# Optimization experiments

Hardware: AMD Instinct MI355X
Metric: run time of the kernel (lower is better)

Reference implementation:

```python
import jax, jax.numpy as jnp
import numpy as np

B, N, M = 8, 8192, 2048
C1, C2 = 128, 256
H = 256  # mlp hidden/out channels


def setup_inputs() -> dict:
    key = jax.random.key(0)
    ks = jax.random.split(key, 8)
    return {
        "unknown": jax.random.normal(ks[0], (B, N, 3), dtype=jnp.float32),
        "known": jax.random.normal(ks[1], (B, M, 3), dtype=jnp.float32),
        "unknow_feats": jax.random.normal(ks[2], (B, C1, N), dtype=jnp.float32),
        "known_feats": jax.random.normal(ks[3], (B, C2, M), dtype=jnp.float32),
        "W1": jax.random.normal(ks[4], (H, C1 + C2), dtype=jnp.float32) * 0.02,
        "b1": jnp.zeros((H,), dtype=jnp.float32),
        "W2": jax.random.normal(ks[5], (H, H), dtype=jnp.float32) * 0.02,
        "b2": jnp.zeros((H,), dtype=jnp.float32),
    }


def _three_nn(unknown, known):
    # squared pairwise distances (B, n, m)
    d2 = jnp.sum((unknown[:, :, None, :] - known[:, None, :, :]) ** 2, axis=-1)
    neg_d2_top, idx = jax.lax.top_k(-d2, 3)  # 3 smallest distances
    dist = jnp.sqrt(jnp.maximum(-neg_d2_top, 0.0))  # (B, n, 3)
    return dist, idx


def _three_interpolate(features, idx, weight):
    # features: (B, c, m); idx, weight: (B, n, 3) -> (B, c, n)
    Bc, c, m = features.shape
    n = idx.shape[1]
    idx_flat = jnp.broadcast_to(idx.reshape(Bc, 1, n * 3), (Bc, c, n * 3))
    gathered = jnp.take_along_axis(features, idx_flat, axis=2).reshape(Bc, c, n, 3)
    return jnp.sum(gathered * weight[:, None, :, :], axis=-1)


def reference(unknown, known, unknow_feats, known_feats, W1, b1, W2, b2):
    dist, idx = _three_nn(unknown, known)
    dist_recip = 1.0 / (dist + 1e-8)
    weight = dist_recip / jnp.sum(dist_recip, axis=2, keepdims=True)  # (B, n, 3)
    interpolated = _three_interpolate(known_feats, idx, weight)  # (B, C2, n)
    new_features = jnp.concatenate([interpolated, unknow_feats], axis=1)  # (B, C1+C2, n)
    # shared MLP: two conv1x1 (bias, no BN) + ReLU
    h = jax.nn.relu(jnp.einsum('oc,bcn->bon', W1, new_features) + b1[None, :, None])
    out = jax.nn.relu(jnp.einsum('oc,bcn->bon', W2, h) + b2[None, :, None])
    return out
```

## Files before the change

kernel.cpp:

```cpp
#include <hip/hip_runtime.h>

using bf16x8 = __attribute__((ext_vector_type(8))) short;
using f32x4  = __attribute__((ext_vector_type(4))) float;

constexpr int Bb = 8, Nn = 8192, Mm = 2048, C1 = 128, C2 = 256, Hh = 256, K1 = 384;
constexpr int KT1 = K1 / 32;
constexpr int KT2 = Hh / 32;
constexpr int RT = Hh / 16;
constexpr int NQ = 2;
constexpr int MQ = Mm / NQ;
constexpr int PSTR = 8;

__device__ __forceinline__ short f2bf(float x) {
  union { float f; unsigned u; } v; v.f = x;
  unsigned r = v.u + 0x7fff + ((v.u >> 16) & 1);
  return (short)(r >> 16);
}

__device__ __forceinline__ unsigned pk2bf(float a, float b) {
#if defined(__has_builtin) && __has_builtin(__builtin_amdgcn_cvt_pk_bf16_f32)
  typedef __attribute__((ext_vector_type(2))) __bf16 bf2_t;
  bf2_t r = __builtin_amdgcn_cvt_pk_bf16_f32(a, b);
  union { bf2_t v; unsigned u; } cvt; cvt.v = r;
  return cvt.u;
#else
  return (unsigned)(unsigned short)f2bf(a) | ((unsigned)(unsigned short)f2bf(b) << 16);
#endif
}

__device__ __forceinline__ float bflo(unsigned d) { return __uint_as_float(d << 16); }
__device__ __forceinline__ float bfhi(unsigned d) { return __uint_as_float(d & 0xffff0000u); }

__device__ __forceinline__ void merge3(float a0, float a1, float a2, int A0, int A1, int A2,
                                       float b0, float b1, float b2, int B0, int B1, int B2,
                                       float& m0, float& m1, float& m2,
                                       int& j0, int& j1, int& j2) {
  bool ta = a0 <= b0;
  m0 = ta ? a0 : b0; j0 = ta ? A0 : B0;
  float na0 = ta ? a1 : a0, na1 = ta ? a2 : a1;
  int   nA0 = ta ? A1 : A0, nA1 = ta ? A2 : A1;
  float nb0 = ta ? b0 : b1, nb1 = ta ? b1 : b2;
  int   nB0 = ta ? B0 : B1, nB1 = ta ? B1 : B2;
  ta = na0 <= nb0;
  m1 = ta ? na0 : nb0; j1 = ta ? nA0 : nB0;
  float ma0 = ta ? na1 : na0; int mA0 = ta ? nA1 : nA0;
  float mb0 = ta ? nb0 : nb1; int mB0 = ta ? nB0 : nB1;
  ta = ma0 <= mb0;
  m2 = ta ? ma0 : mb0; j2 = ta ? mA0 : mB0;
}

__global__ __launch_bounds__(256) void prep_all_k(const float* __restrict__ kf,
                                                  short* __restrict__ kfTb,
                                                  const float* __restrict__ W1,
                                                  const float* __restrict__ W2,
                                                  short* __restrict__ W1f,
                                                  short* __restrict__ W2f) {
  __shared__ float tile[32][33];
  int bid = blockIdx.x, tid = threadIdx.x;
  if (bid < 4096) {
    int cx = bid & 63, ry = (bid >> 6) & 7, z = bid >> 9;
    const float* src = kf + (size_t)z * C2 * Mm;
    short* dst = kfTb + (size_t)z * Mm * C2;
    int c0 = cx * 32, r0 = ry * 32;
    int tx = tid & 31, ty = tid >> 5;
#pragma unroll
    for (int rr = ty; rr < 32; rr += 8)
      tile[rr][tx] = src[(size_t)(r0 + rr) * Mm + c0 + tx];
    __syncthreads();
#pragma unroll
    for (int cc = ty; cc < 32; cc += 8)
      dst[(size_t)(c0 + cc) * C2 + r0 + tx] = f2bf(tile[tx][cc]);
    return;
  }
  int id = (bid - 4096) * 256 + tid;
  const int n1 = KT1 * RT * 64;
  const int n2 = KT2 * RT * 64;
  if (id < n1) {
    int lane = id & 63, t = id >> 6;
    int kt = t / RT, rt = t % RT;
    int m = rt * 16 + (lane & 15), k0 = kt * 32 + (lane >> 4) * 8;
    bf16x8 f;
#pragma unroll
    for (int j = 0; j < 8; ++j) f[j] = f2bf(W1[(size_t)m * K1 + k0 + j]);
    *(bf16x8*)(W1f + (size_t)id * 8) = f;
  } else if (id < n1 + n2) {
    int id2 = id - n1;
    int lane = id2 & 63, t = id2 >> 6;
    int kt = t / RT, rt = t % RT;
    int m = rt * 16 + (lane & 15), k0 = kt * 32 + (lane >> 4) * 8;
    bf16x8 f;
#pragma unroll
    for (int j = 0; j < 8; ++j) f[j] = f2bf(W2[(size_t)m * Hh + k0 + j]);
    *(bf16x8*)(W2f + (size_t)id2 * 8) = f;
  }
}

__global__ __launch_bounds__(256) void nn_half_k(const float* __restrict__ unknown,
                                                 const float* __restrict__ known,
                                                 float* __restrict__ pd,
                                                 int* __restrict__ pi) {
  __shared__ float kx[MQ], ky[MQ], kz[MQ];
  int bid = blockIdx.x;
  int b = bid >> 6, rem = bid & 63;
  int q = rem & 1, nblk = rem >> 1;
  int n = nblk * 256 + threadIdx.x;
  const float* kb = known + ((size_t)b * Mm + q * MQ) * 3;
  for (int p = threadIdx.x; p < MQ; p += 256) {
    kx[p] = kb[3 * p]; ky[p] = kb[3 * p + 1]; kz[p] = kb[3 * p + 2];
  }
  __syncthreads();

  size_t ui = ((size_t)b * Nn + n) * 3;
  float ux = unknown[ui], uy = unknown[ui + 1], uz = unknown[ui + 2];
  float d0 = 1e30f, d1 = 1e30f, d2 = 1e30f;
  int i0 = 0, i1 = 0, i2 = 0;
  int gbase = q * MQ;

#define NN_STEP(xx, yy, zz, qq)                                         \
  {                                                                     \
    float dx = ux - (xx), dy = uy - (yy), dz = uz - (zz);               \
    float dd = dx * dx + dy * dy + dz * dz;                             \
    if (__any(dd < d2)) {    \
      int jm = gbase + jb + (qq);                                       \
      bool c0 = dd < d0, c1 = dd < d1, c2 = dd < d2;                    \
      d2 = c1 ? d1 : (c2 ? dd : d2); i2 = c1 ? i1 : (c2 ? jm : i2);     \
      d1 = c0 ? d0 : (c1 ? dd : d1); i1 = c0 ? i0 : (c1 ? jm : i1);     \
      d0 = c0 ? dd : d0;             i0 = c0 ? jm : i0;                 \
    }                                                                   \
  }

  for (int jb = 0; jb < MQ; jb += 4) {
    float4 xs = *(const float4*)&kx[jb];
    float4 ys = *(const float4*)&ky[jb];
    float4 zs = *(const float4*)&kz[jb];
    NN_STEP(xs.x, ys.x, zs.x, 0)
    NN_STEP(xs.y, ys.y, zs.y, 1)
    NN_STEP(xs.z, ys.z, zs.z, 2)
    NN_STEP(xs.w, ys.w, zs.w, 3)
  }
#undef NN_STEP

  size_t o = ((size_t)b * Nn + n) * PSTR + q * 4;
  *(float4*)&pd[o] = make_float4(d0, d1, d2, 0.f);
  *(int4*)&pi[o]   = make_int4(i0, i1, i2, 0);
}

__global__ __launch_bounds__(256) void fused_gemm_k(
    const float* __restrict__ uf, const short* __restrict__ kfTb,
    const short* __restrict__ W1f, const float* __restrict__ b1,
    const short* __restrict__ W2f, const float* __restrict__ b2,
    const float* __restrict__ pd, const int* __restrict__ pi,
    float* __restrict__ out) {
  __shared__ short Fs[KT1 * 4 * 64 * 8];
  short* Hs = Fs;
  int bid = blockIdx.x;
  int b = bid >> 7, bt = bid & 127;
  int tid = threadIdx.x, lane = tid & 63, wv = tid >> 6;
  int quad = lane >> 4, col = lane & 15;

  {
    int n = bt * 64 + wv * 16 + col;
    size_t pbase = (size_t)(b * Nn + n) * PSTR;
    float4 da = *(const float4*)&pd[pbase];
    float4 db = *(const float4*)&pd[pbase + 4];
    int4 ia = *(const int4*)&pi[pbase];
    int4 ib = *(const int4*)&pi[pbase + 4];
    float m0, m1, m2;
    int g0, g1, g2;
    merge3(da.x, da.y, da.z, ia.x, ia.y, ia.z,
           db.x, db.y, db.z, ib.x, ib.y, ib.z, m0, m1, m2, g0, g1, g2);
    float s0 = sqrtf(m0), s1 = sqrtf(m1), s2 = sqrtf(m2);
    float r0 = 1.f / (s0 + 1e-8f), r1 = 1.f / (s1 + 1e-8f), r2 = 1.f / (s2 + 1e-8f);
    float rs = 1.f / (r0 + r1 + r2);
    float w0 = r0 * rs, w1 = r1 * rs, w2 = r2 * rs;

    const short* kfb = kfTb + (size_t)b * Mm * C2;
#pragma unroll 4
    for (int kt = 0; kt < 8; ++kt) {
      int c0 = kt * 32 + quad * 8;
      uint4 q0 = *(const uint4*)&kfb[(size_t)g0 * C2 + c0];
      uint4 q1 = *(const uint4*)&kfb[(size_t)g1 * C2 + c0];
      uint4 q2 = *(const uint4*)&kfb[(size_t)g2 * C2 + c0];
      float e0 = w0 * bflo(q0.x) + w1 * bflo(q1.x) + w2 * bflo(q2.x);
      float e1 = w0 * bfhi(q0.x) + w1 * bfhi(q1.x) + w2 * bfhi(q2.x);
      float e2 = w0 * bflo(q0.y) + w1 * bflo(q1.y) + w2 * bflo(q2.y);
      float e3 = w0 * bfhi(q0.y) + w1 * bfhi(q1.y) + w2 * bfhi(q2.y);
      float e4 = w0 * bflo(q0.z) + w1 * bflo(q1.z) + w2 * bflo(q2.z);
      float e5 = w0 * bfhi(q0.z) + w1 * bfhi(q1.z) + w2 * bfhi(q2.z);
      float e6 = w0 * bflo(q0.w) + w1 * bflo(q1.w) + w2 * bflo(q2.w);
      float e7 = w0 * bfhi(q0.w) + w1 * bfhi(q1.w) + w2 * bfhi(q2.w);
      uint4 packed;
      packed.x = pk2bf(e0, e1); packed.y = pk2bf(e2, e3);
      packed.z = pk2bf(e4, e5); packed.w = pk2bf(e6, e7);
      *(uint4*)&Fs[((kt * 4 + wv) * 64 + lane) * 8] = packed;
    }
#pragma unroll 2
    for (int kt = 8; kt < 12; ++kt) {
      int c1 = (kt - 8) * 32 + quad * 8;
      float e[8];
#pragma unroll
      for (int j = 0; j < 8; ++j)
        e[j] = uf[((size_t)b * C1 + c1 + j) * Nn + n];
      uint4 packed;
      packed.x = pk2bf(e[0], e[1]); packed.y = pk2bf(e[2], e[3]);
      packed.z = pk2bf(e[4], e[5]); packed.w = pk2bf(e[6], e[7]);
      *(uint4*)&Fs[((kt * 4 + wv) * 64 + lane) * 8] = packed;
    }
  }
  __syncthreads();

  f32x4 acc[4][4];
#pragma unroll
  for (int r = 0; r < 4; ++r)
#pragma unroll
    for (int c = 0; c < 4; ++c) acc[r][c] = (f32x4){0.f, 0.f, 0.f, 0.f};

  for (int kt = 0; kt < KT1; ++kt) {
    bf16x8 Afr[4], Bfr[4];
#pragma unroll
    for (int r = 0; r < 4; ++r)
      Afr[r] = *(const bf16x8*)(W1f + ((size_t)(kt * RT + wv * 4 + r) * 64 + lane) * 8);
#pragma unroll
    for (int c = 0; c < 4; ++c)
      Bfr[c] = *(const bf16x8*)&Fs[((kt * 4 + c) * 64 + lane) * 8];
#pragma unroll
    for (int r = 0; r < 4; ++r)
#pragma unroll
      for (int c = 0; c < 4; ++c)
        acc[r][c] = __builtin_amdgcn_mfma_f32_16x16x32_bf16(Afr[r], Bfr[c], acc[r][c], 0, 0, 0);
  }
  __syncthreads();

#pragma unroll
  for (int r = 0; r < 4; ++r) {
    f32x4 bq = *(const f32x4*)&b1[wv * 64 + r * 16 + quad * 4];
#pragma unroll
    for (int c = 0; c < 4; ++c)
#pragma unroll
      for (int reg = 0; reg < 4; ++reg)
        acc[r][c][reg] = fmaxf(acc[r][c][reg] + bq[reg], 0.f);
  }
  {
    int addr_lo = (((quad & 1) * 2) * 16 + col) * 4;
    bool hiSel = lane >= 32;
#pragma unroll
    for (int ktl = 0; ktl < 2; ++ktl)
#pragma unroll
      for (int c = 0; c < 4; ++c) {
        float e[8];
#pragma unroll
        for (int j = 0; j < 8; ++j) {
          int addr = addr_lo + (j >> 2) * 64;
          int lo = __builtin_amdgcn_ds_bpermute(addr, __float_as_int(acc[ktl * 2][c][j & 3]));
          int hi = __builtin_amdgcn_ds_bpermute(addr, __float_as_int(acc[ktl * 2 + 1][c][j & 3]));
          e[j] = __int_as_float(hiSel ? hi : lo);
        }
        uint4 packed;
        packed.x = pk2bf(e[0], e[1]); packed.y = pk2bf(e[2], e[3]);
        packed.z = pk2bf(e[4], e[5]); packed.w = pk2bf(e[6], e[7]);
        *(uint4*)&Hs[(((wv * 2 + ktl) * 4 + c) * 64 + lane) * 8] = packed;
      }
  }
  __syncthreads();

  f32x4 acc2[4][4];
#pragma unroll
  for (int r = 0; r < 4; ++r)
#pragma unroll
    for (int c = 0; c < 4; ++c) acc2[r][c] = (f32x4){0.f, 0.f, 0.f, 0.f};

  for (int kt = 0; kt < KT2; ++kt) {
    bf16x8 Afr[4], Bfr[4];
#pragma unroll
    for (int r = 0; r < 4; ++r)
      Afr[r] = *(const bf16x8*)(W2f + ((size_t)(kt * RT + wv * 4 + r) * 64 + lane) * 8);
#pragma unroll
    for (int c = 0; c < 4; ++c)
      Bfr[c] = *(const bf16x8*)&Hs[((kt * 4 + c) * 64 + lane) * 8];
#pragma unroll
    for (int r = 0; r < 4; ++r)
#pragma unroll
      for (int c = 0; c < 4; ++c)
        acc2[r][c] = __builtin_amdgcn_mfma_f32_16x16x32_bf16(Afr[r], Bfr[c], acc2[r][c], 0, 0, 0);
  }

#pragma unroll
  for (int r = 0; r < 4; ++r) {
    f32x4 bq = *(const f32x4*)&b2[wv * 64 + r * 16 + quad * 4];
#pragma unroll
    for (int c = 0; c < 4; ++c)
#pragma unroll
      for (int reg = 0; reg < 4; ++reg) {
        int rowg = wv * 64 + r * 16 + quad * 4 + reg;
        int n = bt * 64 + c * 16 + col;
        out[((size_t)b * Hh + rowg) * Nn + n] = fmaxf(acc2[r][c][reg] + bq[reg], 0.f);
      }
  }
}

extern "C" void kernel_launch(void* const* d_in, const int* in_sizes, int n_in,
                              void* d_out, int out_size, void* d_ws, size_t ws_size,
                              hipStream_t stream) {
  const float* unknown = (const float*)d_in[0];
  const float* known   = (const float*)d_in[1];
  const float* uf      = (const float*)d_in[2];
  const float* kf      = (const float*)d_in[3];
  const float* W1      = (const float*)d_in[4];
  const float* b1      = (const float*)d_in[5];
  const float* W2      = (const float*)d_in[6];
  const float* b2      = (const float*)d_in[7];
  float* out = (float*)d_out;

  char* p = (char*)d_ws;
  short* kfTb = (short*)p; p += (size_t)Bb * Mm * C2 * 2;
  short* W1f = (short*)p;  p += (size_t)KT1 * RT * 64 * 8 * 2;
  short* W2f = (short*)p;  p += (size_t)KT2 * RT * 64 * 8 * 2;
  float* pd  = (float*)p;  p += (size_t)Bb * Nn * PSTR * 4;
  int* pi    = (int*)p;    p += (size_t)Bb * Nn * PSTR * 4;

  const int prep_blocks = 4096 + (KT1 * RT * 64 + KT2 * RT * 64 + 255) / 256;
  prep_all_k<<<dim3(prep_blocks), dim3(256), 0, stream>>>(kf, kfTb, W1, W2, W1f, W2f);
  nn_half_k<<<dim3(Bb * 32 * NQ), dim3(256), 0, stream>>>(unknown, known, pd, pi);
  fused_gemm_k<<<dim3(Bb * (Nn / 64)), dim3(256), 0, stream>>>(
      uf, kfTb, W1f, b1, W2f, b2, pd, pi, out);
}
```

Measured before the change: 231.1 us.

## Split nearest-neighbor search into quarters with packed-f32 distance math

The three-NN kernel now splits the known points into four chunks instead of two, which doubles the block count to 1024 and fills the GPU better. Each block stages a smaller slice of coordinates in LDS. Squared distances are computed two at a time with inline-asm v_pk_add/mul/fma_f32 to cut VALU instruction count. Partial top-3 results are stored tightly packed (12 floats per point), and the GEMM kernel now merges four partial lists with three merge3 calls. The costs are more partial-result traffic, extra merge work, and unaligned scalar stores.

```diff
diff --git a/kernel.cpp b/kernel.cpp
--- a/kernel.cpp
+++ b/kernel.cpp
@@ -2,14 +2,14 @@
 
 using bf16x8 = __attribute__((ext_vector_type(8))) short;
 using f32x4  = __attribute__((ext_vector_type(4))) float;
+using f32x2  = __attribute__((ext_vector_type(2))) float;
 
 constexpr int Bb = 8, Nn = 8192, Mm = 2048, C1 = 128, C2 = 256, Hh = 256, K1 = 384;
 constexpr int KT1 = K1 / 32;
 constexpr int KT2 = Hh / 32;
 constexpr int RT = Hh / 16;
-constexpr int NQ = 2;
+constexpr int NQ = 4;
 constexpr int MQ = Mm / NQ;
-constexpr int PSTR = 8;
 
 __device__ __forceinline__ short f2bf(float x) {
   union { float f; unsigned u; } v; v.f = x;
@@ -30,6 +30,16 @@
 
 __device__ __forceinline__ float bflo(unsigned d) { return __uint_as_float(d << 16); }
 __device__ __forceinline__ float bfhi(unsigned d) { return __uint_as_float(d & 0xffff0000u); }
+
+__device__ __forceinline__ f32x2 pk_add(f32x2 a, f32x2 b) {
+  f32x2 d; asm("v_pk_add_f32 %0, %1, %2" : "=v"(d) : "v"(a), "v"(b)); return d;
+}
+__device__ __forceinline__ f32x2 pk_mul(f32x2 a, f32x2 b) {
+  f32x2 d; asm("v_pk_mul_f32 %0, %1, %2" : "=v"(d) : "v"(a), "v"(b)); return d;
+}
+__device__ __forceinline__ f32x2 pk_fma(f32x2 a, f32x2 b, f32x2 c) {
+  f32x2 d; asm("v_pk_fma_f32 %0, %1, %2, %3" : "=v"(d) : "v"(a), "v"(b), "v"(c)); return d;
+}
 
 __device__ __forceinline__ void merge3(float a0, float a1, float a2, int A0, int A1, int A2,
                                        float b0, float b1, float b2, int B0, int B1, int B2,
@@ -95,14 +105,14 @@
   }
 }
 
-__global__ __launch_bounds__(256) void nn_half_k(const float* __restrict__ unknown,
-                                                 const float* __restrict__ known,
-                                                 float* __restrict__ pd,
-                                                 int* __restrict__ pi) {
+__global__ __launch_bounds__(256) void nn_quarter_k(const float* __restrict__ unknown,
+                                                    const float* __restrict__ known,
+                                                    float* __restrict__ pd,
+                                                    int* __restrict__ pi) {
   __shared__ float kx[MQ], ky[MQ], kz[MQ];
   int bid = blockIdx.x;
-  int b = bid >> 6, rem = bid & 63;
-  int q = rem & 1, nblk = rem >> 1;
+  int b = bid >> 7, rem = bid & 127;
+  int q = rem & 3, nblk = rem >> 2;
   int n = nblk * 256 + threadIdx.x;
   const float* kb = known + ((size_t)b * Mm + q * MQ) * 3;
   for (int p = threadIdx.x; p < MQ; p += 256) {
@@ -116,33 +126,41 @@
   int i0 = 0, i1 = 0, i2 = 0;
   int gbase = q * MQ;
 
-#define NN_STEP(xx, yy, zz, qq)                                         \
+  f32x2 nux = { -ux, -ux }, nuy = { -uy, -uy }, nuz = { -uz, -uz };
+
+#define NN_INS(dd, qq)                                                  \
   {                                                                     \
-    float dx = ux - (xx), dy = uy - (yy), dz = uz - (zz);               \
-    float dd = dx * dx + dy * dy + dz * dz;                             \
-    if (__any(dd < d2)) {    \
+    if (__any((dd) < d2)) {  \
       int jm = gbase + jb + (qq);                                       \
-      bool c0 = dd < d0, c1 = dd < d1, c2 = dd < d2;                    \
-      d2 = c1 ? d1 : (c2 ? dd : d2); i2 = c1 ? i1 : (c2 ? jm : i2);     \
-      d1 = c0 ? d0 : (c1 ? dd : d1); i1 = c0 ? i0 : (c1 ? jm : i1);     \
-      d0 = c0 ? dd : d0;             i0 = c0 ? jm : i0;                 \
+      bool c0 = (dd) < d0, c1 = (dd) < d1, c2 = (dd) < d2;              \
+      d2 = c1 ? d1 : (c2 ? (dd) : d2); i2 = c1 ? i1 : (c2 ? jm : i2);   \
+      d1 = c0 ? d0 : (c1 ? (dd) : d1); i1 = c0 ? i0 : (c1 ? jm : i1);   \
+      d0 = c0 ? (dd) : d0;             i0 = c0 ? jm : i0;               \
     }                                                                   \
   }
 
+  const f32x2* kx2 = (const f32x2*)kx;
+  const f32x2* ky2 = (const f32x2*)ky;
+  const f32x2* kz2 = (const f32x2*)kz;
   for (int jb = 0; jb < MQ; jb += 4) {
-    float4 xs = *(const float4*)&kx[jb];
-    float4 ys = *(const float4*)&ky[jb];
-    float4 zs = *(const float4*)&kz[jb];
-    NN_STEP(xs.x, ys.x, zs.x, 0)
-    NN_STEP(xs.y, ys.y, zs.y, 1)
-    NN_STEP(xs.z, ys.z, zs.z, 2)
-    NN_STEP(xs.w, ys.w, zs.w, 3)
-  }
-#undef NN_STEP
-
-  size_t o = ((size_t)b * Nn + n) * PSTR + q * 4;
-  *(float4*)&pd[o] = make_float4(d0, d1, d2, 0.f);
-  *(int4*)&pi[o]   = make_int4(i0, i1, i2, 0);
+    int h = jb >> 1;
+    f32x2 xa = kx2[h], xb = kx2[h + 1];
+    f32x2 ya = ky2[h], yb = ky2[h + 1];
+    f32x2 za = kz2[h], zb = kz2[h + 1];
+    f32x2 dxa = pk_add(xa, nux), dya = pk_add(ya, nuy), dza = pk_add(za, nuz);
+    f32x2 dda = pk_fma(dza, dza, pk_fma(dya, dya, pk_mul(dxa, dxa)));
+    f32x2 dxb = pk_add(xb, nux), dyb = pk_add(yb, nuy), dzb = pk_add(zb, nuz);
+    f32x2 ddb = pk_fma(dzb, dzb, pk_fma(dyb, dyb, pk_mul(dxb, dxb)));
+    NN_INS(dda.x, 0)
+    NN_INS(dda.y, 1)
+    NN_INS(ddb.x, 2)
+    NN_INS(ddb.y, 3)
+  }
+#undef NN_INS
+
+  size_t o = (((size_t)b * Nn + n) * NQ + q) * 3;
+  pd[o] = d0; pd[o + 1] = d1; pd[o + 2] = d2;
+  pi[o] = i0; pi[o + 1] = i1; pi[o + 2] = i2;
 }
 
 __global__ __launch_bounds__(256) void fused_gemm_k(
@@ -160,15 +178,21 @@
 
   {
     int n = bt * 64 + wv * 16 + col;
-    size_t pbase = (size_t)(b * Nn + n) * PSTR;
+    size_t pbase = (size_t)(b * Nn + n) * (NQ * 3);
     float4 da = *(const float4*)&pd[pbase];
     float4 db = *(const float4*)&pd[pbase + 4];
+    float4 dc = *(const float4*)&pd[pbase + 8];
     int4 ia = *(const int4*)&pi[pbase];
     int4 ib = *(const int4*)&pi[pbase + 4];
-    float m0, m1, m2;
-    int g0, g1, g2;
+    int4 ic = *(const int4*)&pi[pbase + 8];
+    float t0, t1, t2, u0, u1, u2, m0, m1, m2;
+    int T0, T1, T2, U0, U1, U2, g0, g1, g2;
     merge3(da.x, da.y, da.z, ia.x, ia.y, ia.z,
-           db.x, db.y, db.z, ib.x, ib.y, ib.z, m0, m1, m2, g0, g1, g2);
+           da.w, db.x, db.y, ia.w, ib.x, ib.y, t0, t1, t2, T0, T1, T2);
+    merge3(db.z, db.w, dc.x, ib.z, ib.w, ic.x,
+           dc.y, dc.z, dc.w, ic.y, ic.z, ic.w, u0, u1, u2, U0, U1, U2);
+    merge3(t0, t1, t2, T0, T1, T2, u0, u1, u2, U0, U1, U2,
+           m0, m1, m2, g0, g1, g2);
     float s0 = sqrtf(m0), s1 = sqrtf(m1), s2 = sqrtf(m2);
     float r0 = 1.f / (s0 + 1e-8f), r1 = 1.f / (s1 + 1e-8f), r2 = 1.f / (s2 + 1e-8f);
     float rs = 1.f / (r0 + r1 + r2);
@@ -315,12 +339,12 @@
   short* kfTb = (short*)p; p += (size_t)Bb * Mm * C2 * 2;
   short* W1f = (short*)p;  p += (size_t)KT1 * RT * 64 * 8 * 2;
   short* W2f = (short*)p;  p += (size_t)KT2 * RT * 64 * 8 * 2;
-  float* pd  = (float*)p;  p += (size_t)Bb * Nn * PSTR * 4;
-  int* pi    = (int*)p;    p += (size_t)Bb * Nn * PSTR * 4;
+  float* pd  = (float*)p;  p += (size_t)Bb * Nn * NQ * 3 * 4;
+  int* pi    = (int*)p;    p += (size_t)Bb * Nn * NQ * 3 * 4;
 
   const int prep_blocks = 4096 + (KT1 * RT * 64 + KT2 * RT * 64 + 255) / 256;
   prep_all_k<<<dim3(prep_blocks), dim3(256), 0, stream>>>(kf, kfTb, W1, W2, W1f, W2f);
-  nn_half_k<<<dim3(Bb * 32 * NQ), dim3(256), 0, stream>>>(unknown, known, pd, pi);
+  nn_quarter_k<<<dim3(Bb * 32 * NQ), dim3(256), 0, stream>>>(unknown, known, pd, pi);
   fused_gemm_k<<<dim3(Bb * (Nn / 64)), dim3(256), 0, stream>>>(
       uf, kfTb, W1f, b1, W2f, b2, pd, pi, out);
 }
```

Measured after the change: 217.1 us. -6.1%, faster.
